# Performance work log

Hardware: AMD Instinct MI355X
Metric: run time of the kernel (lower is better)

## Reference

```python
import jax, jax.numpy as jnp
import numpy as np

N, K, D = 50000, 16, 128
EPS = 1e-5

def _linear_params(key, fan_in, shape_w, shape_b):
    k1, k2 = jax.random.split(key)
    s = 1.0 / np.sqrt(fan_in)
    W = jax.random.uniform(k1, shape_w, minval=-s, maxval=s, dtype=jnp.float32)
    b = jax.random.uniform(k2, shape_b, minval=-s, maxval=s, dtype=jnp.float32)
    return W, b

def setup_inputs() -> dict:
    key = jax.random.key(0)
    ks = jax.random.split(key, 9)
    Wh, bh = _linear_params(ks[0], D, (D, D), (D,))
    Wt, bt = _linear_params(ks[1], D, (D, D), (D,))
    W1, b1 = _linear_params(ks[2], D, (D, D), (D,))
    W2, b2 = _linear_params(ks[3], D, (D, D), (D,))
    return {
        "x": jax.random.normal(ks[4], (N, D), dtype=jnp.float32),
        "e_h_input": jax.random.normal(ks[5], (N, D), dtype=jnp.float32),
        "e_t_input": jax.random.normal(ks[6], (N, D), dtype=jnp.float32),
        "topk_indices": jax.random.randint(ks[7], (N, K), 0, N),
        "topk_weights": jax.random.uniform(ks[8], (N, K), dtype=jnp.float32),
        "Wh": Wh, "bh": bh, "Wt": Wt, "bt": bt,
        "W1": W1, "b1": b1, "W2": W2, "b2": b2,
        "gamma": jnp.ones((D,), jnp.float32),
        "beta": jnp.zeros((D,), jnp.float32),
    }

def reference(x, e_h_input, e_t_input, topk_indices, topk_weights,
              Wh, bh, Wt, bt, W1, b1, W2, b2, gamma, beta):
    e_h = e_h_input @ Wh.T + bh            # [N, D]
    e_t = e_t_input @ Wt.T + bt            # [N, D]
    Nb_h = e_t[topk_indices]               # [N, K, D] neighbor gather
    p = topk_weights[..., None]            # [N, K, 1]
    e_h_exp = e_h[:, None, :]              # [N, 1, D]
    eh_r = p * Nb_h + (1.0 - p) * e_h_exp  # gated mix
    gate = jnp.tanh(e_h_exp + eh_r)
    ka_prob = jax.nn.softmax(jnp.sum(Nb_h * gate, axis=-1), axis=-1)  # [N, K]
    e_Nh = jnp.einsum('nk,nkd->nd', ka_prob, Nb_h)                    # [N, D]
    sum_emb = jax.nn.leaky_relu((x + e_Nh) @ W1.T + b1, 0.01)
    bi_emb = jax.nn.leaky_relu((x * e_Nh) @ W2.T + b2, 0.01)
    h = sum_emb + bi_emb                   # dropout is identity in eval
    mu = jnp.mean(h, axis=-1, keepdims=True)
    var = jnp.var(h, axis=-1, keepdims=True)
    return (h - mu) / jnp.sqrt(var + EPS) * gamma + beta
```

## Files before the change

### kernel.cpp

```cpp
#include <hip/hip_runtime.h>
#include <stdint.h>

#define NROWS 50000
#define KNB 16
#define DD 128
#define LN_EPS 1e-5f

typedef unsigned short ushort_t;
using frag_ab = __attribute__((ext_vector_type(8))) short;
using frag_cd = __attribute__((ext_vector_type(4))) float;

static __device__ __forceinline__ float bf2f(uint32_t u) {
    union { uint32_t i; float f; } v; v.i = u << 16; return v.f;
}
static __device__ __forceinline__ ushort_t f2bf(float f) {
    union { float f; uint32_t i; } v; v.f = f;
    uint32_t x = v.i;
    return (ushort_t)((x + 0x7fffu + ((x >> 16) & 1u)) >> 16);
}
static __device__ __forceinline__ uint32_t packbf(float a, float b) {
    return (uint32_t)f2bf(a) | ((uint32_t)f2bf(b) << 16);
}
static __device__ __forceinline__ float leaky(float v) {
    return v > 0.0f ? v : 0.01f * v;
}
static __device__ __forceinline__ float tanh_fast(float z) {
    float e = __expf(2.0f * z);
    return 1.0f - 2.0f / (e + 1.0f);
}
static __device__ __forceinline__ void split_bf(float f, ushort_t& hi, ushort_t& lo) {
    hi = f2bf(f);
    lo = f2bf(f - bf2f(hi));
}

__global__ __launch_bounds__(256) void linear_mfma2(
    const float* __restrict__ inA, const float* __restrict__ WA,
    const float* __restrict__ bA, float* __restrict__ outA,
    const float* __restrict__ inB, const float* __restrict__ WB,
    const float* __restrict__ bB, float* __restrict__ outB, int nblk)
{
    const int which = blockIdx.x >= nblk;
    const int bid   = which ? blockIdx.x - nblk : blockIdx.x;
    const float* in   = which ? inB : inA;
    const float* W    = which ? WB  : WA;
    const float* bias = which ? bB  : bA;
    float* out        = which ? outB : outA;

    __shared__ ushort_t Wl[128 * 136];
    const int tid = threadIdx.x;
    for (int i = tid; i < 128 * 64; i += 256) {
        int row = i >> 6, cp = (i & 63) << 1;
        float2 w = *(const float2*)(W + row * 128 + cp);
        *(uint32_t*)(&Wl[row * 136 + cp]) = packbf(w.x, w.y);
    }
    const int wv = tid >> 6, lane = tid & 63;
    const int quad = lane >> 4, lq = lane & 15;
    float bn[8];
    #pragma unroll
    for (int nt = 0; nt < 8; ++nt) bn[nt] = bias[nt * 16 + lq];
    __syncthreads();

    const int r0 = bid * 64 + wv * 16;
    const int arow = r0 + lq;
    const int arc = arow < NROWS ? arow : NROWS - 1;

    frag_ab Ahi[4], Alo[4];
    const float* ip = in + (size_t)arc * DD + quad * 8;
    #pragma unroll
    for (int c = 0; c < 4; ++c) {
        float4 u = *(const float4*)(ip + c * 32);
        float4 v = *(const float4*)(ip + c * 32 + 4);
        float uu[8] = {u.x, u.y, u.z, u.w, v.x, v.y, v.z, v.w};
        #pragma unroll
        for (int i = 0; i < 8; ++i) {
            ushort_t h, l; split_bf(uu[i], h, l);
            Ahi[c][i] = (short)h; Alo[c][i] = (short)l;
        }
    }

    #pragma unroll
    for (int nt = 0; nt < 8; ++nt) {
        frag_cd acc = {0.f, 0.f, 0.f, 0.f};
        #pragma unroll
        for (int c = 0; c < 4; ++c) {
            frag_ab B = *(const frag_ab*)(&Wl[(nt * 16 + lq) * 136 + c * 32 + quad * 8]);
            acc = __builtin_amdgcn_mfma_f32_16x16x32_bf16(Alo[c], B, acc, 0, 0, 0);
            acc = __builtin_amdgcn_mfma_f32_16x16x32_bf16(Ahi[c], B, acc, 0, 0, 0);
        }
        #pragma unroll
        for (int r = 0; r < 4; ++r) {
            int orow = r0 + quad * 4 + r;
            if (orow < NROWS)
                out[(size_t)orow * DD + nt * 16 + lq] = acc[r] + bn[nt];
        }
    }
}

__global__ __launch_bounds__(256, 3) void mega_kernel(
    const float* e_h, const float* __restrict__ e_t,
    const int* __restrict__ topk_idx, const float* __restrict__ topk_w,
    const float* __restrict__ x,
    const float* __restrict__ W1, const float* __restrict__ b1,
    const float* __restrict__ W2, const float* __restrict__ b2,
    const float* __restrict__ gamma, const float* __restrict__ beta,
    float* out, int niters)
{
    __shared__ ushort_t aHi[16][136], aLo[16][136];
    __shared__ ushort_t mHi[16][136], mLo[16][136];
    __shared__ float hL[16][132];

    const int tid  = threadIdx.x;
    const int wv   = tid >> 6;
    const int lane = tid & 63;
    const int quad = lane >> 4, lq = lane & 15;
    const int n0   = wv * 32;

    frag_ab BW1[2][4], BW2[2][4];
    #pragma unroll
    for (int t = 0; t < 2; ++t) {
        const float* r1 = W1 + (size_t)(n0 + t * 16 + lq) * DD + quad * 8;
        const float* r2 = W2 + (size_t)(n0 + t * 16 + lq) * DD + quad * 8;
        #pragma unroll
        for (int c = 0; c < 4; ++c) {
            float4 u = *(const float4*)(r1 + c * 32);
            float4 v = *(const float4*)(r1 + c * 32 + 4);
            float uu[8] = {u.x, u.y, u.z, u.w, v.x, v.y, v.z, v.w};
            #pragma unroll
            for (int i = 0; i < 8; ++i) BW1[t][c][i] = (short)f2bf(uu[i]);
            float4 p = *(const float4*)(r2 + c * 32);
            float4 q = *(const float4*)(r2 + c * 32 + 4);
            float vv[8] = {p.x, p.y, p.z, p.w, q.x, q.y, q.z, q.w};
            #pragma unroll
            for (int i = 0; i < 8; ++i) BW2[t][c][i] = (short)f2bf(vv[i]);
        }
    }
    float b1v[2], b2v[2];
    #pragma unroll
    for (int t = 0; t < 2; ++t) {
        b1v[t] = b1[n0 + t * 16 + lq];
        b2v[t] = b2[n0 + t * 16 + lq];
    }
    const float g0 = gamma[lane], g1 = gamma[lane + 64];
    const float be0 = beta[lane], be1 = beta[lane + 64];

    for (int c = blockIdx.x; c < niters; c += gridDim.x) {
        const int r0 = c << 4;

        #pragma unroll
        for (int q = 0; q < 4; ++q) {
            const int lr = 4 * wv + q;
            const int nu = __builtin_amdgcn_readfirstlane(r0 + lr);
            int   tk[KNB];
            float pk[KNB];
            #pragma unroll
            for (int k = 0; k < KNB; ++k) tk[k] = topk_idx[nu * KNB + k];
            #pragma unroll
            for (int k = 0; k < KNB; ++k) pk[k] = topk_w[nu * KNB + k];
            float2 nb[KNB];
            #pragma unroll
            for (int k = 0; k < KNB; ++k) {
                int t = tk[k];
                t = ((unsigned)t < (unsigned)NROWS) ? t : 0;
                nb[k] = *(const float2*)(e_t + (size_t)t * DD + 2 * lane);
            }
            const float2 ehv = *(const float2*)(e_h + (size_t)nu * DD + 2 * lane);
            const float2 xv  = *(const float2*)(x   + (size_t)nu * DD + 2 * lane);

            const float e2x = ehv.x + ehv.x, e2y = ehv.y + ehv.y;

            float s[KNB];
            #pragma unroll
            for (int k = 0; k < KNB; ++k) {
                const float p = pk[k];
                const float ax = __builtin_fmaf(p, nb[k].x - ehv.x, e2x);
                const float ay = __builtin_fmaf(p, nb[k].y - ehv.y, e2y);
                float part = nb[k].x * tanh_fast(ax)
                           + nb[k].y * tanh_fast(ay);
                #pragma unroll
                for (int off = 32; off >= 1; off >>= 1)
                    part += __shfl_xor(part, off, 64);
                s[k] = part;
            }
            float mx = s[0];
            #pragma unroll
            for (int k = 1; k < KNB; ++k) mx = fmaxf(mx, s[k]);
            float sum = 0.0f;
            #pragma unroll
            for (int k = 0; k < KNB; ++k) { s[k] = __expf(s[k] - mx); sum += s[k]; }
            const float inv = 1.0f / sum;
            float e0 = 0.0f, e1 = 0.0f;
            #pragma unroll
            for (int k = 0; k < KNB; ++k) { e0 += s[k] * nb[k].x; e1 += s[k] * nb[k].y; }
            e0 *= inv; e1 *= inv;

            const float a0 = xv.x + e0, a1 = xv.y + e1;
            const float m0 = xv.x * e0, m1 = xv.y * e1;
            ushort_t h0, l0, h1, l1;
            split_bf(a0, h0, l0); split_bf(a1, h1, l1);
            *(uint32_t*)(&aHi[lr][2 * lane]) = (uint32_t)h0 | ((uint32_t)h1 << 16);
            *(uint32_t*)(&aLo[lr][2 * lane]) = (uint32_t)l0 | ((uint32_t)l1 << 16);
            split_bf(m0, h0, l0); split_bf(m1, h1, l1);
            *(uint32_t*)(&mHi[lr][2 * lane]) = (uint32_t)h0 | ((uint32_t)h1 << 16);
            *(uint32_t*)(&mLo[lr][2 * lane]) = (uint32_t)l0 | ((uint32_t)l1 << 16);
        }
        __syncthreads();

        {
            frag_cd aA0 = {0.f,0.f,0.f,0.f}, aA1 = {0.f,0.f,0.f,0.f};
            frag_cd aM0 = {0.f,0.f,0.f,0.f}, aM1 = {0.f,0.f,0.f,0.f};
            #pragma unroll
            for (int kc = 0; kc < 4; ++kc) {
                frag_ab Ah = *(const frag_ab*)(&aHi[lq][kc * 32 + quad * 8]);
                frag_ab Al = *(const frag_ab*)(&aLo[lq][kc * 32 + quad * 8]);
                frag_ab Mh = *(const frag_ab*)(&mHi[lq][kc * 32 + quad * 8]);
                frag_ab Ml = *(const frag_ab*)(&mLo[lq][kc * 32 + quad * 8]);
                aA0 = __builtin_amdgcn_mfma_f32_16x16x32_bf16(Al, BW1[0][kc], aA0, 0, 0, 0);
                aA0 = __builtin_amdgcn_mfma_f32_16x16x32_bf16(Ah, BW1[0][kc], aA0, 0, 0, 0);
                aA1 = __builtin_amdgcn_mfma_f32_16x16x32_bf16(Al, BW1[1][kc], aA1, 0, 0, 0);
                aA1 = __builtin_amdgcn_mfma_f32_16x16x32_bf16(Ah, BW1[1][kc], aA1, 0, 0, 0);
                aM0 = __builtin_amdgcn_mfma_f32_16x16x32_bf16(Ml, BW2[0][kc], aM0, 0, 0, 0);
                aM0 = __builtin_amdgcn_mfma_f32_16x16x32_bf16(Mh, BW2[0][kc], aM0, 0, 0, 0);
                aM1 = __builtin_amdgcn_mfma_f32_16x16x32_bf16(Ml, BW2[1][kc], aM1, 0, 0, 0);
                aM1 = __builtin_amdgcn_mfma_f32_16x16x32_bf16(Mh, BW2[1][kc], aM1, 0, 0, 0);
            }
            #pragma unroll
            for (int r = 0; r < 4; ++r) {
                const int row = quad * 4 + r;
                hL[row][n0 + lq]      = leaky(aA0[r] + b1v[0]) + leaky(aM0[r] + b2v[0]);
                hL[row][n0 + 16 + lq] = leaky(aA1[r] + b1v[1]) + leaky(aM1[r] + b2v[1]);
            }
        }
        __syncthreads();

        #pragma unroll
        for (int q = 0; q < 4; ++q) {
            const int lr = 4 * wv + q;
            const float h0 = hL[lr][lane], h1 = hL[lr][lane + 64];
            float s = h0 + h1, qq = h0 * h0 + h1 * h1;
            #pragma unroll
            for (int off = 32; off >= 1; off >>= 1) {
                s  += __shfl_xor(s,  off, 64);
                qq += __shfl_xor(qq, off, 64);
            }
            const float mu  = s * (1.0f / DD);
            const float var = qq * (1.0f / DD) - mu * mu;
            const float rs  = rsqrtf(var + LN_EPS);
            out[(size_t)(r0 + lr) * DD + lane]      = (h0 - mu) * rs * g0 + be0;
            out[(size_t)(r0 + lr) * DD + lane + 64] = (h1 - mu) * rs * g1 + be1;
        }
        __syncthreads();
    }
}

extern "C" void kernel_launch(void* const* d_in, const int* in_sizes, int n_in,
                              void* d_out, int out_size, void* d_ws, size_t ws_size,
                              hipStream_t stream) {
    const float* x      = (const float*)d_in[0];
    const float* ehi    = (const float*)d_in[1];
    const float* eti    = (const float*)d_in[2];
    const int*   tidx   = (const int*)d_in[3];
    const float* tw     = (const float*)d_in[4];
    const float* Wh     = (const float*)d_in[5];
    const float* bh     = (const float*)d_in[6];
    const float* Wt     = (const float*)d_in[7];
    const float* bt     = (const float*)d_in[8];
    const float* W1     = (const float*)d_in[9];
    const float* b1     = (const float*)d_in[10];
    const float* W2     = (const float*)d_in[11];
    const float* b2     = (const float*)d_in[12];
    const float* gamma  = (const float*)d_in[13];
    const float* beta   = (const float*)d_in[14];

    float* e_h = (float*)d_out;
    float* e_t = (float*)d_ws;

    const int nblk = (NROWS + 63) / 64;

    linear_mfma2<<<2 * nblk, 256, 0, stream>>>(ehi, Wh, bh, e_h,
                                               eti, Wt, bt, e_t, nblk);
    mega_kernel<<<1563, 256, 0, stream>>>(e_h, e_t, tidx, tw, x,
                                          W1, b1, W2, b2, gamma, beta,
                                          (float*)d_out, NROWS / 16);
}
```

Baseline: 307.8 us.

## Reload W1/W2 fragments per iteration to cut registers and raise occupancy

Weight fragments for W1 and W2 are no longer held in registers for the whole persistent loop. Each iteration now reloads them from global memory (L1/L2-resident) and converts them with the packed bf16 conversion instruction. The freed registers allow the launch bound to rise from 3 to 4 blocks per SM, and the grid shrinks to 1024 persistent blocks. The cost is repeated global loads and conversions of weights on every 16-row tile, in exchange for more waves to hide the gather latency.

Measured after the change: 269.8 us. 12.4% less time.

```diff
diff --git a/kernel.cpp b/kernel.cpp
--- a/kernel.cpp
+++ b/kernel.cpp
@@ -31,6 +31,21 @@
 static __device__ __forceinline__ void split_bf(float f, ushort_t& hi, ushort_t& lo) {
     hi = f2bf(f);
     lo = f2bf(f - bf2f(hi));
+}
+static __device__ __forceinline__ uint32_t cvtpk(float lo, float hi) {
+    uint32_t r;
+    asm("v_cvt_pk_bf16_f32 %0, %1, %2" : "=v"(r) : "v"(lo), "v"(hi));
+    return r;
+}
+static __device__ __forceinline__ frag_ab load_wfrag(const float* wp) {
+    float4 u = *(const float4*)(wp);
+    float4 v = *(const float4*)(wp + 4);
+    union { uint32_t d[4]; frag_ab f; } r;
+    r.d[0] = cvtpk(u.x, u.y);
+    r.d[1] = cvtpk(u.z, u.w);
+    r.d[2] = cvtpk(v.x, v.y);
+    r.d[3] = cvtpk(v.z, v.w);
+    return r.f;
 }
 
 __global__ __launch_bounds__(256) void linear_mfma2(
@@ -96,12 +111,12 @@
     }
 }
 
-__global__ __launch_bounds__(256, 3) void mega_kernel(
+__global__ __launch_bounds__(256, 4) void mega_kernel(
     const float* e_h, const float* __restrict__ e_t,
     const int* __restrict__ topk_idx, const float* __restrict__ topk_w,
     const float* __restrict__ x,
-    const float* __restrict__ W1, const float* __restrict__ b1,
-    const float* __restrict__ W2, const float* __restrict__ b2,
+    const float* W1, const float* __restrict__ b1,
+    const float* W2, const float* __restrict__ b2,
     const float* __restrict__ gamma, const float* __restrict__ beta,
     float* out, int niters)
 {
@@ -115,25 +130,6 @@
     const int quad = lane >> 4, lq = lane & 15;
     const int n0   = wv * 32;
 
-    frag_ab BW1[2][4], BW2[2][4];
-    #pragma unroll
-    for (int t = 0; t < 2; ++t) {
-        const float* r1 = W1 + (size_t)(n0 + t * 16 + lq) * DD + quad * 8;
-        const float* r2 = W2 + (size_t)(n0 + t * 16 + lq) * DD + quad * 8;
-        #pragma unroll
-        for (int c = 0; c < 4; ++c) {
-            float4 u = *(const float4*)(r1 + c * 32);
-            float4 v = *(const float4*)(r1 + c * 32 + 4);
-            float uu[8] = {u.x, u.y, u.z, u.w, v.x, v.y, v.z, v.w};
-            #pragma unroll
-            for (int i = 0; i < 8; ++i) BW1[t][c][i] = (short)f2bf(uu[i]);
-            float4 p = *(const float4*)(r2 + c * 32);
-            float4 q = *(const float4*)(r2 + c * 32 + 4);
-            float vv[8] = {p.x, p.y, p.z, p.w, q.x, q.y, q.z, q.w};
-            #pragma unroll
-            for (int i = 0; i < 8; ++i) BW2[t][c][i] = (short)f2bf(vv[i]);
-        }
-    }
     float b1v[2], b2v[2];
     #pragma unroll
     for (int t = 0; t < 2; ++t) {
@@ -142,6 +138,9 @@
     }
     const float g0 = gamma[lane], g1 = gamma[lane + 64];
     const float be0 = beta[lane], be1 = beta[lane + 64];
+
+    const float* w1p = W1 + (size_t)(n0 + lq) * DD + quad * 8;
+    const float* w2p = W2 + (size_t)(n0 + lq) * DD + quad * 8;
 
     for (int c = blockIdx.x; c < niters; c += gridDim.x) {
         const int r0 = c << 4;
@@ -210,18 +209,22 @@
             frag_cd aM0 = {0.f,0.f,0.f,0.f}, aM1 = {0.f,0.f,0.f,0.f};
             #pragma unroll
             for (int kc = 0; kc < 4; ++kc) {
+                frag_ab B10 = load_wfrag(w1p + kc * 32);
+                frag_ab B11 = load_wfrag(w1p + 16 * DD + kc * 32);
+                frag_ab B20 = load_wfrag(w2p + kc * 32);
+                frag_ab B21 = load_wfrag(w2p + 16 * DD + kc * 32);
                 frag_ab Ah = *(const frag_ab*)(&aHi[lq][kc * 32 + quad * 8]);
                 frag_ab Al = *(const frag_ab*)(&aLo[lq][kc * 32 + quad * 8]);
                 frag_ab Mh = *(const frag_ab*)(&mHi[lq][kc * 32 + quad * 8]);
                 frag_ab Ml = *(const frag_ab*)(&mLo[lq][kc * 32 + quad * 8]);
-                aA0 = __builtin_amdgcn_mfma_f32_16x16x32_bf16(Al, BW1[0][kc], aA0, 0, 0, 0);
-                aA0 = __builtin_amdgcn_mfma_f32_16x16x32_bf16(Ah, BW1[0][kc], aA0, 0, 0, 0);
-                aA1 = __builtin_amdgcn_mfma_f32_16x16x32_bf16(Al, BW1[1][kc], aA1, 0, 0, 0);
-                aA1 = __builtin_amdgcn_mfma_f32_16x16x32_bf16(Ah, BW1[1][kc], aA1, 0, 0, 0);
-                aM0 = __builtin_amdgcn_mfma_f32_16x16x32_bf16(Ml, BW2[0][kc], aM0, 0, 0, 0);
-                aM0 = __builtin_amdgcn_mfma_f32_16x16x32_bf16(Mh, BW2[0][kc], aM0, 0, 0, 0);
-                aM1 = __builtin_amdgcn_mfma_f32_16x16x32_bf16(Ml, BW2[1][kc], aM1, 0, 0, 0);
-                aM1 = __builtin_amdgcn_mfma_f32_16x16x32_bf16(Mh, BW2[1][kc], aM1, 0, 0, 0);
+                aA0 = __builtin_amdgcn_mfma_f32_16x16x32_bf16(Al, B10, aA0, 0, 0, 0);
+                aA0 = __builtin_amdgcn_mfma_f32_16x16x32_bf16(Ah, B10, aA0, 0, 0, 0);
+                aA1 = __builtin_amdgcn_mfma_f32_16x16x32_bf16(Al, B11, aA1, 0, 0, 0);
+                aA1 = __builtin_amdgcn_mfma_f32_16x16x32_bf16(Ah, B11, aA1, 0, 0, 0);
+                aM0 = __builtin_amdgcn_mfma_f32_16x16x32_bf16(Ml, B20, aM0, 0, 0, 0);
+                aM0 = __builtin_amdgcn_mfma_f32_16x16x32_bf16(Mh, B20, aM0, 0, 0, 0);
+                aM1 = __builtin_amdgcn_mfma_f32_16x16x32_bf16(Ml, B21, aM1, 0, 0, 0);
+                aM1 = __builtin_amdgcn_mfma_f32_16x16x32_bf16(Mh, B21, aM1, 0, 0, 0);
             }
             #pragma unroll
             for (int r = 0; r < 4; ++r) {
@@ -278,7 +281,7 @@
 
     linear_mfma2<<<2 * nblk, 256, 0, stream>>>(ehi, Wh, bh, e_h,
                                                eti, Wt, bt, e_t, nblk);
-    mega_kernel<<<1563, 256, 0, stream>>>(e_h, e_t, tidx, tw, x,
+    mega_kernel<<<1024, 256, 0, stream>>>(e_h, e_t, tidx, tw, x,
                                           W1, b1, W2, b2, gamma, beta,
                                           (float*)d_out, NROWS / 16);
 }
```
